# Performance work log

Hardware: AMD Instinct MI355X
Metric: run time of the kernel (lower is better)

## Reference

```python
import jax, jax.numpy as jnp
import numpy as np

B, C, H, W = 4, 256, 64, 64
C8 = C // 8

def setup_inputs() -> dict:
    key = jax.random.key(0)
    ks = jax.random.split(key, 8)
    s = 1.0 / np.sqrt(C)
    return {
        "x": jax.random.normal(ks[0], (B, C, H, W), dtype=jnp.float32),
        "wq": jax.random.normal(ks[1], (C8, C), dtype=jnp.float32) * s,
        "bq": jax.random.normal(ks[2], (C8,), dtype=jnp.float32) * 0.01,
        "wk": jax.random.normal(ks[3], (C8, C), dtype=jnp.float32) * s,
        "bk": jax.random.normal(ks[4], (C8,), dtype=jnp.float32) * 0.01,
        "wv": jax.random.normal(ks[5], (C, C), dtype=jnp.float32) * s,
        "bv": jax.random.normal(ks[6], (C,), dtype=jnp.float32) * 0.01,
        "gamma": jax.random.normal(ks[7], (1,), dtype=jnp.float32) * 0.1,
    }

def reference(x, wq, bq, wk, bk, wv, bv, gamma):
    b, c, h, w = x.shape
    n = h * w
    xf = x.reshape(b, c, n)                       # [B,C,N]
    # 1x1 convs == per-pixel linear projections
    q = jnp.einsum('dc,bcn->bdn', wq, xf) + bq[None, :, None]   # [B,C8,N]
    k = jnp.einsum('dc,bcn->bdn', wk, xf) + bk[None, :, None]   # [B,C8,N]
    v = jnp.einsum('dc,bcn->bdn', wv, xf) + bv[None, :, None]   # [B,C,N]
    energy = jnp.einsum('bdi,bdj->bij', q, k)     # [B,N,N], i=query, j=key
    attn = jax.nn.softmax(energy, axis=-1)
    out = jnp.einsum('bcj,bij->bci', v, attn)     # [B,C,N]
    out = out.reshape(b, c, h, w)
    return gamma * out + x
```

## Files before the change

### kernel.cpp

```cpp
#include <hip/hip_runtime.h>
#include <math.h>

#define BATCH 4
#define CH    256
#define CQK   32
#define NPIX  4096
#define NT    32
#define LOG2E 1.4426950408889634f

typedef __attribute__((ext_vector_type(8))) short short8;
typedef __attribute__((ext_vector_type(4))) float f32x4;

static __device__ __forceinline__ unsigned short f2bf(float f) {
    unsigned u = __builtin_bit_cast(unsigned, f);
    u = (u + 0x7fffu + ((u >> 16) & 1u)) >> 16;
    return (unsigned short)u;
}
static __device__ __forceinline__ float bf2f(unsigned short s) {
    unsigned u = ((unsigned)s) << 16;
    return __builtin_bit_cast(float, u);
}
static __device__ __forceinline__ float exp2_fast(float x) {
    float r; asm("v_exp_f32 %0, %1" : "=v"(r) : "v"(x)); return r;
}
static __device__ __forceinline__ unsigned cvt_pk_bf16(float lo, float hi) {
    unsigned r; asm("v_cvt_pk_bf16_f32 %0, %1, %2" : "=v"(r) : "v"(lo), "v"(hi)); return r;
}

__global__ __launch_bounds__(256) void wcvt_kernel(
    const float* __restrict__ wq, const float* __restrict__ wk,
    const float* __restrict__ wv,
    unsigned short* __restrict__ Wh, unsigned short* __restrict__ Wl)
{
    int idx = blockIdx.x * 256 + threadIdx.x;
    int r = idx >> 8, c = idx & 255;
    float f;
    if (r < 32)       f = wq[r * 256 + c] * LOG2E;
    else if (r < 64)  f = wk[(r - 32) * 256 + c];
    else              f = wv[(r - 64) * 256 + c];
    unsigned short h = f2bf(f);
    Wh[idx] = h;
    Wl[idx] = f2bf(f - bf2f(h));
}

__global__ __launch_bounds__(256) void qkv_kernel(
    const float* __restrict__ x,
    const float* __restrict__ bq, const float* __restrict__ bk,
    const float* __restrict__ bv,
    const unsigned short* __restrict__ Wh, const unsigned short* __restrict__ Wl,
    unsigned short* __restrict__ Qh, unsigned short* __restrict__ Kh,
    unsigned short* __restrict__ Vb)
{
    extern __shared__ char xsmem[];
    char* const Xh = xsmem;
    char* const Xl = xsmem + 32768;

    const int b  = blockIdx.y;
    const int n0 = blockIdx.x * 64;
    const int t  = threadIdx.x;

    #pragma unroll
    for (int rep = 0; rep < 8; ++rep) {
        int idx = rep * 256 + t;
        int cp = idx >> 4, n4 = idx & 15;
        int c = cp * 2;
        float4 a4 = *(const float4*)&x[((size_t)b * CH + c) * NPIX + n0 + n4 * 4];
        float4 b4 = *(const float4*)&x[((size_t)b * CH + c + 1) * NPIX + n0 + n4 * 4];
        #pragma unroll
        for (int u = 0; u < 4; ++u) {
            int n = n4 * 4 + u;
            float fa = (&a4.x)[u], fb = (&b4.x)[u];
            unsigned short ha = f2bf(fa), hb = f2bf(fb);
            unsigned short la = f2bf(fa - bf2f(ha)), lb = f2bf(fb - bf2f(hb));
            int off = n * 512 + (((c >> 3) * 16) ^ ((n & 7) << 4)) + (c & 7) * 2;
            *(unsigned*)(Xh + off) = (unsigned)ha | ((unsigned)hb << 16);
            *(unsigned*)(Xl + off) = (unsigned)la | ((unsigned)lb << 16);
        }
    }
    __syncthreads();

    const int w = t >> 6, l = t & 63, g = l >> 4, m = l & 15;

    for (int dt = 0; dt < 5; ++dt) {
        const int d0 = w * 80 + dt * 16;

        short8 wh[8], wl[8];
        #pragma unroll
        for (int ks = 0; ks < 8; ++ks) {
            size_t off = (size_t)(d0 + m) * 256 + ks * 32 + g * 8;
            wh[ks] = __builtin_bit_cast(short8, *(const uint4*)&Wh[off]);
            wl[ks] = __builtin_bit_cast(short8, *(const uint4*)&Wl[off]);
        }

        f32x4 acc[4];
        #pragma unroll
        for (int nt = 0; nt < 4; ++nt) acc[nt] = (f32x4){0.f, 0.f, 0.f, 0.f};
        #pragma unroll
        for (int nt = 0; nt < 4; ++nt) {
            const int n = nt * 16 + m;
            #pragma unroll
            for (int ks = 0; ks < 8; ++ks) {
                int off = n * 512 + (((ks * 4 + g) * 16) ^ ((n & 7) << 4));
                short8 xh = __builtin_bit_cast(short8, *(const uint4*)(Xh + off));
                short8 xl = __builtin_bit_cast(short8, *(const uint4*)(Xl + off));
                acc[nt] = __builtin_amdgcn_mfma_f32_16x16x32_bf16(wh[ks], xh, acc[nt], 0, 0, 0);
                acc[nt] = __builtin_amdgcn_mfma_f32_16x16x32_bf16(wh[ks], xl, acc[nt], 0, 0, 0);
                acc[nt] = __builtin_amdgcn_mfma_f32_16x16x32_bf16(wl[ks], xh, acc[nt], 0, 0, 0);
            }
        }

        int kind;
        float4 bias;
        if (d0 < 32)      { kind = 0; bias = *(const float4*)&bq[d0 + g * 4];
                            bias.x *= LOG2E; bias.y *= LOG2E; bias.z *= LOG2E; bias.w *= LOG2E; }
        else if (d0 < 64) { kind = 1; bias = *(const float4*)&bk[d0 - 32 + g * 4]; }
        else              { kind = 2; bias = *(const float4*)&bv[d0 - 64 + g * 4]; }

        #pragma unroll
        for (int nt = 0; nt < 4; ++nt) {
            const int n = n0 + nt * 16 + m;
            if (kind == 2) {
                const int c0 = d0 - 64;
                #pragma unroll
                for (int r = 0; r < 4; ++r) {
                    float val = acc[nt][r] + (&bias.x)[r];
                    Vb[((size_t)b * CH + c0 + g * 4 + r) * NPIX + n] = f2bf(val);
                }
            } else {
                unsigned short hs[4];
                #pragma unroll
                for (int r = 0; r < 4; ++r)
                    hs[r] = f2bf(acc[nt][r] + (&bias.x)[r]);
                const int dcol = (d0 & 31) + g * 4;
                const size_t base = ((size_t)b * NPIX + n) * CQK + dcol;
                uint2 uh;
                uh.x = (unsigned)hs[0] | ((unsigned)hs[1] << 16);
                uh.y = (unsigned)hs[2] | ((unsigned)hs[3] << 16);
                if (kind == 0) *(uint2*)&Qh[base] = uh;
                else           *(uint2*)&Kh[base] = uh;
            }
        }
    }
}


#define CONS_STEP(JT, PF) do {                                                 \
    const int _jb   = ((JT) - 1) * 128;                                        \
    const int _pidx = ((JT) & 1) ^ 1;                                          \
    const char* pb = (const char*)Pbuf[_pidx];                                 \
    float ff[4];                                                               \
    _Pragma("unroll")                                                          \
    for (int f = 0; f < 4; ++f) ff[f] = sFac[_pidx][f * 16 + m];               \
    uint4 vB[8];                                                               \
    _Pragma("unroll")                                                          \
    for (int cf = 0; cf < 4; ++cf) {                                           \
        vB[cf * 2]     = *(const uint4*)&vrow[cf][_jb + 64 + g * 8];           \
        vB[cf * 2 + 1] = *(const uint4*)&vrow[cf][_jb + 96 + g * 8];           \
    }                                                                          \
    short8 pf[4][2];                                                           \
    _Pragma("unroll")                                                          \
    for (int f = 0; f < 4; ++f)                                                \
        _Pragma("unroll")                                                      \
        for (int k2 = 0; k2 < 2; ++k2)                                         \
            pf[f][k2] = __builtin_bit_cast(short8, *(const uint4*)(pb +        \
                (f * 16 + m) * 256 + ((k2 * 64 + g * 16) ^ (m << 4))));        \
    if (!__all(ff[0] == 1.f && ff[1] == 1.f && ff[2] == 1.f && ff[3] == 1.f)) { \
        _Pragma("unroll")                                                      \
        for (int cf = 0; cf < 4; ++cf)                                         \
            _Pragma("unroll")                                                  \
            for (int f = 0; f < 4; ++f) acc[cf][f] *= ff[f];                   \
    }                                                                          \
    _Pragma("unroll")                                                          \
    for (int cf = 0; cf < 4; ++cf) {                                           \
        short8 v0 = __builtin_bit_cast(short8, vAc[cf * 2]);                   \
        short8 v1 = __builtin_bit_cast(short8, vAc[cf * 2 + 1]);               \
        _Pragma("unroll")                                                      \
        for (int f = 0; f < 4; ++f) {                                          \
            f32x4 a = acc[cf][f];                                              \
            a = __builtin_amdgcn_mfma_f32_16x16x32_bf16(v0, pf[f][0], a, 0, 0, 0); \
            a = __builtin_amdgcn_mfma_f32_16x16x32_bf16(v1, pf[f][1], a, 0, 0, 0); \
            acc[cf][f] = a;                                                    \
        }                                                                      \
    }                                                                          \
    if (PF) {                                                                  \
        _Pragma("unroll")                                                      \
        for (int cf = 0; cf < 4; ++cf) {                                       \
            vAc[cf * 2]     = *(const uint4*)&vrow[cf][_jb + 128 + g * 8];     \
            vAc[cf * 2 + 1] = *(const uint4*)&vrow[cf][_jb + 160 + g * 8];     \
        }                                                                      \
    }                                                                          \
    short8 pg[4][2];                                                           \
    _Pragma("unroll")                                                          \
    for (int f = 0; f < 4; ++f)                                                \
        _Pragma("unroll")                                                      \
        for (int k2 = 0; k2 < 2; ++k2)                                         \
            pg[f][k2] = __builtin_bit_cast(short8, *(const uint4*)(pb +        \
                (f * 16 + m) * 256 + (((k2 + 2) * 64 + g * 16) ^ (m << 4))));  \
    _Pragma("unroll")                                                          \
    for (int cf = 0; cf < 4; ++cf) {                                           \
        short8 v0 = __builtin_bit_cast(short8, vB[cf * 2]);                    \
        short8 v1 = __builtin_bit_cast(short8, vB[cf * 2 + 1]);                \
        _Pragma("unroll")                                                      \
        for (int f = 0; f < 4; ++f) {                                          \
            f32x4 a = acc[cf][f];                                              \
            a = __builtin_amdgcn_mfma_f32_16x16x32_bf16(v0, pg[f][0], a, 0, 0, 0); \
            a = __builtin_amdgcn_mfma_f32_16x16x32_bf16(v1, pg[f][1], a, 0, 0, 0); \
            acc[cf][f] = a;                                                    \
        }                                                                      \
    }                                                                          \
} while (0)

__global__ __launch_bounds__(512, 2) void attn_kernel(
    const unsigned short* __restrict__ Qh, const unsigned short* __restrict__ Kh,
    const unsigned short* __restrict__ Vb,
    const float* __restrict__ x, const float* __restrict__ gamma,
    float* __restrict__ out)
{
    __shared__ __align__(16) char Ksw[2][8192];
    __shared__ __align__(16) uint4 Pbuf[2][1024];
    __shared__ float sFac[2][64];
    __shared__ float sL[64];

    const int bid = blockIdx.x;
    const int b   = (bid & 7) >> 1;
    const int it  = (bid >> 3) + ((bid & 1) << 5);
    const int i0  = it * 64;

    const int t   = threadIdx.x;
    const int wv8 = t >> 6;
    const bool isProd = (wv8 < 4);
    const int w   = wv8 & 3;
    const int l   = t & 63, g = l >> 4, m = l & 15;
    const int irow = w * 16 + m;

    {
        int sj = t >> 2, sq = t & 3;
        int wr = sj * 64 + ((sq * 16) ^ (((sj >> 1) & 3) << 4));
        *(uint4*)&Ksw[0][wr] =
            *(const uint4*)&Kh[((size_t)b * NPIX + sj) * CQK + sq * 8];
    }

    short8 qh = {};
    float m_run = -1e30f, l_run = 0.f;
    if (isProd) {
        const int iq = i0 + irow;
        qh = __builtin_bit_cast(short8, *(const uint4*)&Qh[((size_t)b * NPIX + iq) * CQK + g * 8]);
    }

    f32x4 acc[4][4];
    #pragma unroll
    for (int cf = 0; cf < 4; ++cf)
        #pragma unroll
        for (int f = 0; f < 4; ++f) acc[cf][f] = (f32x4){0.f, 0.f, 0.f, 0.f};
    const unsigned short* vrow[4];
    uint4 vAc[8];
    size_t kpf_base = 0;
    int kwr0 = 0;
    if (!isProd) {
        #pragma unroll
        for (int cf = 0; cf < 4; ++cf)
            vrow[cf] = Vb + ((size_t)b * CH + w * 64 + cf * 16 + m) * NPIX;
        const int t2  = t & 255;
        const int sj0 = t2 >> 2, sq0 = t2 & 3;
        kpf_base = ((size_t)b * NPIX + sj0) * CQK + sq0 * 8;
        kwr0 = sj0 * 64 + ((sq0 * 16) ^ (((sj0 >> 1) & 3) << 4));
        #pragma unroll
        for (int cf = 0; cf < 4; ++cf) {
            vAc[cf * 2]     = *(const uint4*)&vrow[cf][g * 8];
            vAc[cf * 2 + 1] = *(const uint4*)&vrow[cf][32 + g * 8];
        }
    }

    __syncthreads();

    for (int jt = 0; jt < NT; ++jt) {
        const int idx = jt & 1;

        if (isProd) {
            f32x4 sv[8];
            #pragma unroll
            for (int jf = 0; jf < 8; ++jf) {
                short8 kh8 = __builtin_bit_cast(short8,
                    *(const uint4*)&Ksw[idx][jf * 1024 + m * 64 +
                        ((g * 16) ^ (((m >> 1) & 3) << 4))]);
                f32x4 s = (f32x4){0.f, 0.f, 0.f, 0.f};
                s = __builtin_amdgcn_mfma_f32_16x16x32_bf16(kh8, qh, s, 0, 0, 0);
                sv[jf] = s;
            }

            float s32[32];
            #pragma unroll
            for (int jf = 0; jf < 8; ++jf)
                #pragma unroll
                for (int r = 0; r < 4; ++r) s32[jf * 4 + r] = sv[jf][r];

            float mx[16];
            #pragma unroll
            for (int k = 0; k < 16; ++k) mx[k] = fmaxf(s32[k], s32[k + 16]);
            #pragma unroll
            for (int k = 0; k < 8; ++k) mx[k] = fmaxf(mx[k], mx[k + 8]);
            #pragma unroll
            for (int k = 0; k < 4; ++k) mx[k] = fmaxf(mx[k], mx[k + 4]);
            float tmax = fmaxf(fmaxf(mx[0], mx[2]), fmaxf(mx[1], mx[3]));

            float fac = 1.0f;
            if (!__all(tmax <= m_run + 11.5f)) {
                float tc = fmaxf(tmax, __shfl_xor(tmax, 16));
                tc = fmaxf(tc, __shfl_xor(tc, 32));
                float mt = fmaxf(m_run, tc);
                fac = exp2_fast(m_run - mt);
                m_run = mt;
            }

            float p[32];
            #pragma unroll
            for (int k = 0; k < 32; ++k) p[k] = exp2_fast(s32[k] - m_run);
            float sm[16];
            #pragma unroll
            for (int k = 0; k < 16; ++k) sm[k] = p[k] + p[k + 16];
            #pragma unroll
            for (int k = 0; k < 8; ++k) sm[k] = sm[k] + sm[k + 8];
            #pragma unroll
            for (int k = 0; k < 4; ++k) sm[k] = sm[k] + sm[k + 4];
            float tsum = (sm[0] + sm[2]) + (sm[1] + sm[3]);
            tsum += __shfl_xor(tsum, 16);
            tsum += __shfl_xor(tsum, 32);
            l_run = l_run * fac + tsum;
            if (g == 0) sFac[idx][irow] = fac;

            char* pb = (char*)Pbuf[idx];
            #pragma unroll
            for (int jf = 0; jf < 8; ++jf) {
                uint2 u;
                u.x = cvt_pk_bf16(p[jf * 4 + 0], p[jf * 4 + 1]);
                u.y = cvt_pk_bf16(p[jf * 4 + 2], p[jf * 4 + 3]);
                *(uint2*)(pb + irow * 256 + ((jf * 32 + g * 8) ^ (m << 4))) = u;
            }
        } else {
            const bool doK = (jt < NT - 1);
            uint4 pk0, pk1;
            if (doK) {
                const size_t rb = kpf_base + (size_t)((jt + 1) * 128) * CQK;
                pk0 = *(const uint4*)&Kh[rb];
                pk1 = *(const uint4*)&Kh[rb + 2048];
            }

            if (jt >= 1) CONS_STEP(jt, true);

            if (doK) {
                *(uint4*)&Ksw[idx ^ 1][kwr0] = pk0;
                *(uint4*)&Ksw[idx ^ 1][kwr0 + 4096] = pk1;
            }
        }

        __syncthreads();
    }

    if (isProd) {
        if (g == 0) sL[irow] = l_run;
    }
    __syncthreads();
    if (!isProd) {
        CONS_STEP(NT, false);
        const float gm = gamma[0];
        #pragma unroll
        for (int f = 0; f < 4; ++f) {
            float linv = 1.0f / sL[f * 16 + m];
            #pragma unroll
            for (int cf = 0; cf < 4; ++cf) {
                #pragma unroll
                for (int r = 0; r < 4; ++r) {
                    int c = w * 64 + cf * 16 + g * 4 + r;
                    size_t o = ((size_t)b * CH + c) * NPIX + i0 + f * 16 + m;
                    out[o] = gm * acc[cf][f][r] * linv + x[o];
                }
            }
        }
    }
}

extern "C" void kernel_launch(void* const* d_in, const int* in_sizes, int n_in,
                              void* d_out, int out_size, void* d_ws, size_t ws_size,
                              hipStream_t stream) {
    const float* x     = (const float*)d_in[0];
    const float* wq    = (const float*)d_in[1];
    const float* bq    = (const float*)d_in[2];
    const float* wk    = (const float*)d_in[3];
    const float* bk    = (const float*)d_in[4];
    const float* wv    = (const float*)d_in[5];
    const float* bv    = (const float*)d_in[6];
    const float* gamma = (const float*)d_in[7];
    float* out = (float*)d_out;

    unsigned short* base = (unsigned short*)d_ws;
    const size_t qk_sz = (size_t)BATCH * NPIX * CQK;
    unsigned short* Qh = base;
    unsigned short* Kh = Qh + qk_sz;
    unsigned short* Vb = Kh + qk_sz;
    unsigned short* Wh = Vb + (size_t)BATCH * CH * NPIX;
    unsigned short* Wl = Wh + 320 * 256;

    wcvt_kernel<<<320, 256, 0, stream>>>(wq, wk, wv, Wh, Wl);
    qkv_kernel<<<dim3(64, 4), 256, 65536, stream>>>(x, bq, bk, bv, Wh, Wl,
                                                    Qh, Kh, Vb);
    attn_kernel<<<256, 512, 0, stream>>>(Qh, Kh, Vb, x, gamma, out);
}
```

Measured before the change: 102.0 us.

## Process two key tiles per barrier with 4-deep K/P ring buffers

Restructures the producer/consumer attention loop so each iteration handles two 128-key tiles, using four-slot LDS ring buffers for K and P in dynamic shared memory. K global prefetch is pushed two tiles ahead, and the block-wide __syncthreads is replaced by an lgkmcnt-only wait plus s_barrier, which halves barrier count and avoids waiting on outstanding global loads. It raises LDS use to about 97KB and adds register pressure from the double V and K prefetch buffers, which may limit occupancy.

```diff
diff --git a/kernel.cpp b/kernel.cpp
--- a/kernel.cpp
+++ b/kernel.cpp
@@ -25,6 +25,10 @@
 }
 static __device__ __forceinline__ unsigned cvt_pk_bf16(float lo, float hi) {
     unsigned r; asm("v_cvt_pk_bf16_f32 %0, %1, %2" : "=v"(r) : "v"(lo), "v"(hi)); return r;
+}
+static __device__ __forceinline__ void barrier_lgkm_only() {
+    asm volatile("s_waitcnt lgkmcnt(0)" ::: "memory");
+    __builtin_amdgcn_s_barrier();
 }
 
 __global__ __launch_bounds__(256) void wcvt_kernel(
@@ -144,13 +148,71 @@
 }
 
 
-#define CONS_STEP(JT, PF) do {                                                 \
-    const int _jb   = ((JT) - 1) * 128;                                        \
-    const int _pidx = ((JT) & 1) ^ 1;                                          \
-    const char* pb = (const char*)Pbuf[_pidx];                                 \
+#define PROD_STEP(S) do {                                                      \
+    const int _idx = (S) & 3;                                                  \
+    const char* kb = Kb + _idx * 8192;                                         \
+    f32x4 sv[8];                                                               \
+    _Pragma("unroll")                                                          \
+    for (int jf = 0; jf < 8; ++jf) {                                           \
+        short8 kh8 = __builtin_bit_cast(short8, *(const uint4*)&kb[            \
+            jf * 1024 + m * 64 + ((g * 16) ^ (((m >> 1) & 3) << 4))]);         \
+        f32x4 s = (f32x4){0.f, 0.f, 0.f, 0.f};                                 \
+        s = __builtin_amdgcn_mfma_f32_16x16x32_bf16(kh8, qh, s, 0, 0, 0);      \
+        sv[jf] = s;                                                            \
+    }                                                                          \
+    float s32[32];                                                             \
+    _Pragma("unroll")                                                          \
+    for (int jf = 0; jf < 8; ++jf)                                             \
+        _Pragma("unroll")                                                      \
+        for (int r = 0; r < 4; ++r) s32[jf * 4 + r] = sv[jf][r];               \
+    float mx[16];                                                              \
+    _Pragma("unroll")                                                          \
+    for (int k = 0; k < 16; ++k) mx[k] = fmaxf(s32[k], s32[k + 16]);           \
+    _Pragma("unroll")                                                          \
+    for (int k = 0; k < 8; ++k) mx[k] = fmaxf(mx[k], mx[k + 8]);               \
+    _Pragma("unroll")                                                          \
+    for (int k = 0; k < 4; ++k) mx[k] = fmaxf(mx[k], mx[k + 4]);               \
+    float tmax = fmaxf(fmaxf(mx[0], mx[2]), fmaxf(mx[1], mx[3]));              \
+    float fac = 1.0f;                                                          \
+    if (!__all(tmax <= m_run + 11.5f)) {                                       \
+        float tc = fmaxf(tmax, __shfl_xor(tmax, 16));                          \
+        tc = fmaxf(tc, __shfl_xor(tc, 32));                                    \
+        float mt = fmaxf(m_run, tc);                                           \
+        fac = exp2_fast(m_run - mt);                                           \
+        m_run = mt;                                                            \
+    }                                                                          \
+    float p[32];                                                               \
+    _Pragma("unroll")                                                          \
+    for (int k = 0; k < 32; ++k) p[k] = exp2_fast(s32[k] - m_run);             \
+    float sm[16];                                                              \
+    _Pragma("unroll")                                                          \
+    for (int k = 0; k < 16; ++k) sm[k] = p[k] + p[k + 16];                     \
+    _Pragma("unroll")                                                          \
+    for (int k = 0; k < 8; ++k) sm[k] = sm[k] + sm[k + 8];                     \
+    _Pragma("unroll")                                                          \
+    for (int k = 0; k < 4; ++k) sm[k] = sm[k] + sm[k + 4];                     \
+    float tsum = (sm[0] + sm[2]) + (sm[1] + sm[3]);                            \
+    tsum += __shfl_xor(tsum, 16);                                              \
+    tsum += __shfl_xor(tsum, 32);                                              \
+    l_run = l_run * fac + tsum;                                                \
+    if (g == 0) sF[_idx * 64 + irow] = fac;                                    \
+    char* pbw = Pb + _idx * 16384;                                             \
+    _Pragma("unroll")                                                          \
+    for (int jf = 0; jf < 8; ++jf) {                                           \
+        uint2 u;                                                               \
+        u.x = cvt_pk_bf16(p[jf * 4 + 0], p[jf * 4 + 1]);                       \
+        u.y = cvt_pk_bf16(p[jf * 4 + 2], p[jf * 4 + 3]);                       \
+        *(uint2*)(pbw + irow * 256 + ((jf * 32 + g * 8) ^ (m << 4))) = u;      \
+    }                                                                          \
+} while (0)
+
+#define CONS_PV(S, VBUF, PF) do {                                              \
+    const int _s  = (S);                                                       \
+    const int _jb = _s * 128;                                                  \
+    const char* pb = Pb + (_s & 3) * 16384;                                    \
     float ff[4];                                                               \
     _Pragma("unroll")                                                          \
-    for (int f = 0; f < 4; ++f) ff[f] = sFac[_pidx][f * 16 + m];               \
+    for (int f = 0; f < 4; ++f) ff[f] = sF[(_s & 3) * 64 + f * 16 + m];        \
     uint4 vB[8];                                                               \
     _Pragma("unroll")                                                          \
     for (int cf = 0; cf < 4; ++cf) {                                           \
@@ -172,8 +234,8 @@
     }                                                                          \
     _Pragma("unroll")                                                          \
     for (int cf = 0; cf < 4; ++cf) {                                           \
-        short8 v0 = __builtin_bit_cast(short8, vAc[cf * 2]);                   \
-        short8 v1 = __builtin_bit_cast(short8, vAc[cf * 2 + 1]);               \
+        short8 v0 = __builtin_bit_cast(short8, VBUF[cf * 2]);                  \
+        short8 v1 = __builtin_bit_cast(short8, VBUF[cf * 2 + 1]);              \
         _Pragma("unroll")                                                      \
         for (int f = 0; f < 4; ++f) {                                          \
             f32x4 a = acc[cf][f];                                              \
@@ -185,8 +247,8 @@
     if (PF) {                                                                  \
         _Pragma("unroll")                                                      \
         for (int cf = 0; cf < 4; ++cf) {                                       \
-            vAc[cf * 2]     = *(const uint4*)&vrow[cf][_jb + 128 + g * 8];     \
-            vAc[cf * 2 + 1] = *(const uint4*)&vrow[cf][_jb + 160 + g * 8];     \
+            VBUF[cf * 2]     = *(const uint4*)&vrow[cf][_jb + 256 + g * 8];    \
+            VBUF[cf * 2 + 1] = *(const uint4*)&vrow[cf][_jb + 288 + g * 8];    \
         }                                                                      \
     }                                                                          \
     short8 pg[4][2];                                                           \
@@ -216,10 +278,11 @@
     const float* __restrict__ x, const float* __restrict__ gamma,
     float* __restrict__ out)
 {
-    __shared__ __align__(16) char Ksw[2][8192];
-    __shared__ __align__(16) uint4 Pbuf[2][1024];
-    __shared__ float sFac[2][64];
-    __shared__ float sL[64];
+    extern __shared__ char smem[];
+    char* const Kb = smem;
+    char* const Pb = smem + 32768;
+    float* const sF = (float*)(smem + 98304);
+    float* const sL = (float*)(smem + 99328);
 
     const int bid = blockIdx.x;
     const int b   = (bid & 7) >> 1;
@@ -236,8 +299,9 @@
     {
         int sj = t >> 2, sq = t & 3;
         int wr = sj * 64 + ((sq * 16) ^ (((sj >> 1) & 3) << 4));
-        *(uint4*)&Ksw[0][wr] =
-            *(const uint4*)&Kh[((size_t)b * NPIX + sj) * CQK + sq * 8];
+        const size_t gb = ((size_t)b * NPIX + sj) * CQK + sq * 8;
+        *(uint4*)&Kb[wr]        = *(const uint4*)&Kh[gb];
+        *(uint4*)&Kb[8192 + wr] = *(const uint4*)&Kh[gb + (size_t)128 * CQK];
     }
 
     short8 qh = {};
@@ -253,7 +317,8 @@
         #pragma unroll
         for (int f = 0; f < 4; ++f) acc[cf][f] = (f32x4){0.f, 0.f, 0.f, 0.f};
     const unsigned short* vrow[4];
-    uint4 vAc[8];
+    uint4 vAc[8], vAd[8];
+    uint4 pkA0 = {}, pkA1 = {}, pkB0 = {}, pkB1 = {};
     size_t kpf_base = 0;
     int kwr0 = 0;
     if (!isProd) {
@@ -268,92 +333,48 @@
         for (int cf = 0; cf < 4; ++cf) {
             vAc[cf * 2]     = *(const uint4*)&vrow[cf][g * 8];
             vAc[cf * 2 + 1] = *(const uint4*)&vrow[cf][32 + g * 8];
-        }
+            vAd[cf * 2]     = *(const uint4*)&vrow[cf][128 + g * 8];
+            vAd[cf * 2 + 1] = *(const uint4*)&vrow[cf][160 + g * 8];
+        }
+        pkA0 = *(const uint4*)&Kh[kpf_base + (size_t)(2 * 128) * CQK];
+        pkA1 = *(const uint4*)&Kh[kpf_base + (size_t)(2 * 128) * CQK + 2048];
+        pkB0 = *(const uint4*)&Kh[kpf_base + (size_t)(3 * 128) * CQK];
+        pkB1 = *(const uint4*)&Kh[kpf_base + (size_t)(3 * 128) * CQK + 2048];
     }
 
     __syncthreads();
 
-    for (int jt = 0; jt < NT; ++jt) {
-        const int idx = jt & 1;
-
+    for (int T = 0; T < NT / 2; ++T) {
         if (isProd) {
-            f32x4 sv[8];
-            #pragma unroll
-            for (int jf = 0; jf < 8; ++jf) {
-                short8 kh8 = __builtin_bit_cast(short8,
-                    *(const uint4*)&Ksw[idx][jf * 1024 + m * 64 +
-                        ((g * 16) ^ (((m >> 1) & 3) << 4))]);
-                f32x4 s = (f32x4){0.f, 0.f, 0.f, 0.f};
-                s = __builtin_amdgcn_mfma_f32_16x16x32_bf16(kh8, qh, s, 0, 0, 0);
-                sv[jf] = s;
-            }
-
-            float s32[32];
-            #pragma unroll
-            for (int jf = 0; jf < 8; ++jf)
-                #pragma unroll
-                for (int r = 0; r < 4; ++r) s32[jf * 4 + r] = sv[jf][r];
-
-            float mx[16];
-            #pragma unroll
-            for (int k = 0; k < 16; ++k) mx[k] = fmaxf(s32[k], s32[k + 16]);
-            #pragma unroll
-            for (int k = 0; k < 8; ++k) mx[k] = fmaxf(mx[k], mx[k + 8]);
-            #pragma unroll
-            for (int k = 0; k < 4; ++k) mx[k] = fmaxf(mx[k], mx[k + 4]);
-            float tmax = fmaxf(fmaxf(mx[0], mx[2]), fmaxf(mx[1], mx[3]));
-
-            float fac = 1.0f;
-            if (!__all(tmax <= m_run + 11.5f)) {
-                float tc = fmaxf(tmax, __shfl_xor(tmax, 16));
-                tc = fmaxf(tc, __shfl_xor(tc, 32));
-                float mt = fmaxf(m_run, tc);
-                fac = exp2_fast(m_run - mt);
-                m_run = mt;
-            }
-
-            float p[32];
-            #pragma unroll
-            for (int k = 0; k < 32; ++k) p[k] = exp2_fast(s32[k] - m_run);
-            float sm[16];
-            #pragma unroll
-            for (int k = 0; k < 16; ++k) sm[k] = p[k] + p[k + 16];
-            #pragma unroll
-            for (int k = 0; k < 8; ++k) sm[k] = sm[k] + sm[k + 8];
-            #pragma unroll
-            for (int k = 0; k < 4; ++k) sm[k] = sm[k] + sm[k + 4];
-            float tsum = (sm[0] + sm[2]) + (sm[1] + sm[3]);
-            tsum += __shfl_xor(tsum, 16);
-            tsum += __shfl_xor(tsum, 32);
-            l_run = l_run * fac + tsum;
-            if (g == 0) sFac[idx][irow] = fac;
-
-            char* pb = (char*)Pbuf[idx];
-            #pragma unroll
-            for (int jf = 0; jf < 8; ++jf) {
-                uint2 u;
-                u.x = cvt_pk_bf16(p[jf * 4 + 0], p[jf * 4 + 1]);
-                u.y = cvt_pk_bf16(p[jf * 4 + 2], p[jf * 4 + 3]);
-                *(uint2*)(pb + irow * 256 + ((jf * 32 + g * 8) ^ (m << 4))) = u;
-            }
+            PROD_STEP(2 * T);
+            PROD_STEP(2 * T + 1);
         } else {
-            const bool doK = (jt < NT - 1);
-            uint4 pk0, pk1;
+            if (T < NT / 2 - 1) {
+                char* ka = Kb + ((2 * T + 2) & 3) * 8192;
+                char* kc = Kb + ((2 * T + 3) & 3) * 8192;
+                *(uint4*)&ka[kwr0] = pkA0;
+                *(uint4*)&ka[kwr0 + 4096] = pkA1;
+                *(uint4*)&kc[kwr0] = pkB0;
+                *(uint4*)&kc[kwr0 + 4096] = pkB1;
+            }
+            uint4 nA0, nA1, nB0, nB1;
+            const bool doK = (T < NT / 2 - 2);
             if (doK) {
-                const size_t rb = kpf_base + (size_t)((jt + 1) * 128) * CQK;
-                pk0 = *(const uint4*)&Kh[rb];
-                pk1 = *(const uint4*)&Kh[rb + 2048];
-            }
-
-            if (jt >= 1) CONS_STEP(jt, true);
-
-            if (doK) {
-                *(uint4*)&Ksw[idx ^ 1][kwr0] = pk0;
-                *(uint4*)&Ksw[idx ^ 1][kwr0 + 4096] = pk1;
-            }
-        }
-
-        __syncthreads();
+                nA0 = *(const uint4*)&Kh[kpf_base + (size_t)((2 * T + 4) * 128) * CQK];
+                nA1 = *(const uint4*)&Kh[kpf_base + (size_t)((2 * T + 4) * 128) * CQK + 2048];
+                nB0 = *(const uint4*)&Kh[kpf_base + (size_t)((2 * T + 5) * 128) * CQK];
+                nB1 = *(const uint4*)&Kh[kpf_base + (size_t)((2 * T + 5) * 128) * CQK + 2048];
+            }
+
+            if (T >= 1) {
+                CONS_PV(2 * T - 2, vAc, true);
+                CONS_PV(2 * T - 1, vAd, true);
+            }
+
+            if (doK) { pkA0 = nA0; pkA1 = nA1; pkB0 = nB0; pkB1 = nB1; }
+        }
+
+        barrier_lgkm_only();
     }
 
     if (isProd) {
@@ -361,7 +382,8 @@
     }
     __syncthreads();
     if (!isProd) {
-        CONS_STEP(NT, false);
+        CONS_PV(NT - 2, vAc, false);
+        CONS_PV(NT - 1, vAd, false);
         const float gm = gamma[0];
         #pragma unroll
         for (int f = 0; f < 4; ++f) {
@@ -403,5 +425,5 @@
     wcvt_kernel<<<320, 256, 0, stream>>>(wq, wk, wv, Wh, Wl);
     qkv_kernel<<<dim3(64, 4), 256, 65536, stream>>>(x, bq, bk, bv, Wh, Wl,
                                                     Qh, Kh, Vb);
-    attn_kernel<<<256, 512, 0, stream>>>(Qh, Kh, Vb, x, gamma, out);
-}
+    attn_kernel<<<256, 512, 99584, stream>>>(Qh, Kh, Vb, x, gamma, out);
+}
```

Measured after the change: 147.6 us. 44.7% more time.
